# Kernel tuning notes

Measured on AMD Instinct MI355X. Metric: run time of the kernel, lower is better.

The kernel has to match this reference:

```python
import jax, jax.numpy as jnp
import numpy as np
import math

NUM_HEADS = 16
CONSTITUENCY_PENALTY = 0.5
CONSTITUENT_BLOCK = 64  # deterministic stand-in for the ChomskyParser constituency spans


def constituency_penalty_mask(seq_len, dtype):
    # Tokens in the same constituent (contiguous block) attend freely;
    # cross-constituent pairs are penalized by CONSTITUENCY_PENALTY.
    blk = jnp.arange(seq_len) // CONSTITUENT_BLOCK
    return jnp.where(blk[:, None] != blk[None, :], CONSTITUENCY_PENALTY, 0.0).astype(dtype)


def setup_inputs() -> dict:
    key = jax.random.key(0)
    ks = jax.random.split(key, 7)
    B, S, H = 8, 1024, 1024
    scale = 1.0 / math.sqrt(H)
    return {
        "hidden_states": jax.random.normal(ks[0], (B, S, H), jnp.float32),
        "Wq": jax.random.normal(ks[1], (H, H), jnp.float32) * scale,
        "bq": jnp.zeros((H,), jnp.float32),
        "Wk": jax.random.normal(ks[2], (H, H), jnp.float32) * scale,
        "bk": jnp.zeros((H,), jnp.float32),
        "Wv": jax.random.normal(ks[3], (H, H), jnp.float32) * scale,
        "bv": jnp.zeros((H,), jnp.float32),
    }


def reference(hidden_states, Wq, bq, Wk, bk, Wv, bv):
    B, S, H = hidden_states.shape
    nh = NUM_HEADS
    hd = H // nh

    def heads(x):  # [B,S,H] -> [B,nh,S,hd]
        return x.reshape(B, S, nh, hd).transpose(0, 2, 1, 3)

    q = heads(hidden_states @ Wq + bq)
    k = heads(hidden_states @ Wk + bk)
    v = heads(hidden_states @ Wv + bv)

    scores = jnp.einsum("bhqd,bhkd->bhqk", q, k) / jnp.sqrt(jnp.asarray(hd, q.dtype))
    # constituency penalty subtracted before softmax (broadcast over batch, heads)
    scores = scores - constituency_penalty_mask(S, scores.dtype)[None, None, :, :]
    probs = jax.nn.softmax(scores, axis=-1)  # dropout is identity in eval

    ctx = jnp.einsum("bhqk,bhkd->bhqd", probs, v)
    ctx = ctx.transpose(0, 2, 1, 3).reshape(B, S, H)
    return ctx
```

## Files before the change

### kernel.cpp

```cpp
#include <hip/hip_runtime.h>
#include <cstdint>

#define BB 8
#define SQ 1024
#define HH 1024
#define NH 16
#define HD 64

typedef __attribute__((ext_vector_type(4))) float f32x4;
typedef __attribute__((ext_vector_type(8))) __bf16 bf16x8;
typedef __attribute__((ext_vector_type(8))) unsigned short u16x8;
typedef __attribute__((ext_vector_type(4))) unsigned short u16x4;

__device__ __forceinline__ unsigned short f2bf(float f){
  uint32_t u = __builtin_bit_cast(uint32_t, f);
  u += 0x7FFFu + ((u >> 16) & 1u);
  return (unsigned short)(u >> 16);
}

__device__ __forceinline__ void gload_lds16(const void* g, void* l){
  __builtin_amdgcn_global_load_lds((__attribute__((address_space(1))) void*)g,
                                   (__attribute__((address_space(3))) void*)l,
                                   16, 0, 0);
}

__global__ __launch_bounds__(256) void k_convert_x(const float* __restrict__ x,
                                                   unsigned short* __restrict__ xb){
  int i = blockIdx.x * 256 + threadIdx.x;
  const f32x4* xv = (const f32x4*)x;
  f32x4 a = xv[2*i], b = xv[2*i+1];
  u16x8 o;
  o[0]=f2bf(a[0]); o[1]=f2bf(a[1]); o[2]=f2bf(a[2]); o[3]=f2bf(a[3]);
  o[4]=f2bf(b[0]); o[5]=f2bf(b[1]); o[6]=f2bf(b[2]); o[7]=f2bf(b[3]);
  ((u16x8*)xb)[i] = o;
}

__global__ __launch_bounds__(256) void k_wt(const float* __restrict__ Wq,
                                            const float* __restrict__ Wk,
                                            const float* __restrict__ Wv,
                                            unsigned short* __restrict__ wt){
  __shared__ float t[32][33];
  int p = blockIdx.z;
  const float* W = (p==0)?Wq:((p==1)?Wk:Wv);
  int n0 = blockIdx.x*32, k0 = blockIdx.y*32;
  int tx = threadIdx.x, ty = threadIdx.y;
  #pragma unroll
  for(int j=0;j<32;j+=8) t[ty+j][tx] = W[(size_t)(k0+ty+j)*HH + n0+tx];
  __syncthreads();
  unsigned short* o = wt + (size_t)p*HH*HH;
  #pragma unroll
  for(int j=0;j<32;j+=8) o[(size_t)(n0+ty+j)*HH + k0+tx] = f2bf(t[tx][ty+j]);
}

#define BM 128
#define BN 128
#define BK 64
__global__ __launch_bounds__(256) void k_qkv(const unsigned short* __restrict__ Xb,
                                             const unsigned short* __restrict__ Wt,
                                             const float* __restrict__ bq,
                                             const float* __restrict__ bk,
                                             const float* __restrict__ bv,
                                             unsigned short* __restrict__ q_ws,
                                             unsigned short* __restrict__ k_ws,
                                             unsigned short* __restrict__ vt_ws){
  __shared__ __align__(16) unsigned short As[2][BM*BK];
  __shared__ __align__(16) unsigned short Bs[2][BN*BK];
  int tid = threadIdx.x;
  int lane = tid & 63, wid = tid >> 6;
  int bid = blockIdx.x;
  int sw = (bid & 7)*192 + (bid >> 3);
  int nt = sw % 24, mt = sw / 24;
  int m0 = mt*BM, n0 = nt*BN;
  int wm = (wid & 1)*64, wn = (wid >> 1)*64;
  int lr = lane & 15, g = lane >> 4;

  int srow = tid >> 3;
  int sch  = (tid & 7) ^ (srow & 7);

  const f32x4 zf = {0.f,0.f,0.f,0.f};
  f32x4 acc[4][4];
  #pragma unroll
  for(int a=0;a<4;a++)
    #pragma unroll
    for(int b=0;b<4;b++) acc[a][b] = zf;

  #pragma unroll
  for(int it=0; it<4; it++){
    int row = it*32 + srow, slot = it*256 + tid;
    gload_lds16(Xb + (size_t)(m0+row)*1024 + sch*8, &As[0][slot*8]);
    gload_lds16(Wt + (size_t)(n0+row)*1024 + sch*8, &Bs[0][slot*8]);
  }
  __syncthreads();

  int cur = 0;
  for(int kk=0; kk<16; kk++){
    if(kk < 15){
      int kb = (kk+1)*BK;
      #pragma unroll
      for(int it=0; it<4; it++){
        int row = it*32 + srow, slot = it*256 + tid;
        gload_lds16(Xb + (size_t)(m0+row)*1024 + kb + sch*8, &As[cur^1][slot*8]);
        gload_lds16(Wt + (size_t)(n0+row)*1024 + kb + sch*8, &Bs[cur^1][slot*8]);
      }
    }
    #pragma unroll
    for(int ks=0; ks<2; ks++){
      bf16x8 af[4], bfr[4];
      #pragma unroll
      for(int mi=0;mi<4;mi++){
        int r = wm + mi*16 + lr;
        af[mi] = *(const bf16x8*)&As[cur][r*64 + (((ks*4+g) ^ (r&7))<<3)];
      }
      #pragma unroll
      for(int ni=0;ni<4;ni++){
        int r = wn + ni*16 + lr;
        bfr[ni] = *(const bf16x8*)&Bs[cur][r*64 + (((ks*4+g) ^ (r&7))<<3)];
      }
      #pragma unroll
      for(int mi=0;mi<4;mi++)
        #pragma unroll
        for(int ni=0;ni<4;ni++)
          acc[mi][ni] = __builtin_amdgcn_mfma_f32_16x16x32_bf16(af[mi], bfr[ni], acc[mi][ni], 0,0,0);
    }
    __syncthreads();
    cur ^= 1;
  }

  int proj = n0 >> 10;
  const float* bias = (proj==0)?bq:((proj==1)?bk:bv);
  const float QSCALE = 0.18033688f;
  #pragma unroll
  for(int mi=0;mi<4;mi++){
    #pragma unroll
    for(int ni=0;ni<4;ni++){
      int ncol = n0 + wn + ni*16 + lr;
      int hcol = ncol & 1023;
      int h = hcol >> 6, d = hcol & 63;
      float bval = bias[hcol];
      if(proj == 0){
        #pragma unroll
        for(int i=0;i<4;i++){
          int m = m0 + wm + mi*16 + g*4 + i;
          int b = m >> 10, s = m & 1023;
          q_ws[((size_t)(b*NH + h)*SQ + s)*HD + d] = f2bf((acc[mi][ni][i] + bval)*QSCALE);
        }
      } else if(proj == 1){
        #pragma unroll
        for(int i=0;i<4;i++){
          int m = m0 + wm + mi*16 + g*4 + i;
          int b = m >> 10, s = m & 1023;
          k_ws[((size_t)(b*NH + h)*SQ + s)*HD + d] = f2bf(acc[mi][ni][i] + bval);
        }
      } else {
        int m = m0 + wm + mi*16 + g*4;
        int b = m >> 10, s = m & 1023;
        u16x4 pk;
        #pragma unroll
        for(int i=0;i<4;i++) pk[i] = f2bf(acc[mi][ni][i] + bval);
        *(u16x4*)&vt_ws[((size_t)(b*NH + h)*HD + d)*SQ + s] = pk;
      }
    }
  }
}

__global__ __launch_bounds__(256) void k_attn(const unsigned short* __restrict__ q_ws,
                                              const unsigned short* __restrict__ k_ws,
                                              const unsigned short* __restrict__ vt_ws,
                                              float* __restrict__ out){
  __shared__ __align__(16) unsigned short Ks[2][64*64];
  __shared__ __align__(16) unsigned short Vs[2][64*64];
  __shared__ __align__(16) unsigned short Ps[4][32*64];
  int tid = threadIdx.x, lane = tid & 63, wid = tid >> 6;
  int lr = lane & 15, g = lane >> 4;
  int bid = blockIdx.x;
  int swz = (bid & 7)*128 + (bid >> 3);
  int qb = swz & 7, bh = swz >> 3;
  int qw = qb*128 + wid*32;
  const unsigned short* qp = q_ws + (size_t)bh*SQ*HD;
  const unsigned short* kp = k_ws + (size_t)bh*SQ*HD;
  const unsigned short* vp = vt_ws + (size_t)bh*HD*SQ;

  bf16x8 qf[2][2];
  #pragma unroll
  for(int ns=0;ns<2;ns++)
    #pragma unroll
    for(int ks=0;ks<2;ks++)
      qf[ns][ks] = *(const bf16x8*)&qp[(size_t)(qw + ns*16 + lr)*HD + ks*32 + g*8];

  int diag = qw >> 6;

  int srow = tid >> 3;
  int sch  = (tid & 7) ^ (srow & 7);

  const f32x4 zf = {0.f,0.f,0.f,0.f};
  float lacc[2] = {0.f, 0.f};
  f32x4 co[4][2];
  #pragma unroll
  for(int ms=0;ms<4;ms++)
    #pragma unroll
    for(int ns=0;ns<2;ns++) co[ms][ns] = zf;

  unsigned short* Pw = &Ps[wid][0];

  #pragma unroll
  for(int it=0; it<2; it++){
    int row = it*32 + srow, slot = it*256 + tid;
    gload_lds16(kp + (size_t)row*HD + sch*8, &Ks[0][slot*8]);
    gload_lds16(vp + (size_t)row*SQ + sch*8, &Vs[0][slot*8]);
  }
  __syncthreads();

  int cur = 0;
  for(int kt=0; kt<16; kt++){
    if(kt < 15){
      int kb = (kt+1)*64;
      #pragma unroll
      for(int it=0; it<2; it++){
        int row = it*32 + srow, slot = it*256 + tid;
        gload_lds16(kp + (size_t)(kb+row)*HD + sch*8, &Ks[cur^1][slot*8]);
        gload_lds16(vp + (size_t)row*SQ + kb + sch*8, &Vs[cur^1][slot*8]);
      }
    }

    f32x4 sc[4][2];
    #pragma unroll
    for(int ms=0;ms<4;ms++){
      int r = ms*16 + lr;
      bf16x8 kf0 = *(const bf16x8*)&Ks[cur][r*64 + ((g ^ (r&7))<<3)];
      bf16x8 kf1 = *(const bf16x8*)&Ks[cur][r*64 + (((4+g) ^ (r&7))<<3)];
      #pragma unroll
      for(int ns=0;ns<2;ns++){
        sc[ms][ns] = __builtin_amdgcn_mfma_f32_16x16x32_bf16(kf0, qf[ns][0], zf, 0,0,0);
        sc[ms][ns] = __builtin_amdgcn_mfma_f32_16x16x32_bf16(kf1, qf[ns][1], sc[ms][ns], 0,0,0);
      }
    }

    float add = (kt == diag) ? 0.72134752f : 0.0f;

    #pragma unroll
    for(int ms=0;ms<4;ms++){
      #pragma unroll
      for(int ns=0;ns<2;ns++){
        u16x4 pk;
        #pragma unroll
        for(int i=0;i<4;i++){
          float pv = __builtin_amdgcn_exp2f(sc[ms][ns][i] + add);
          lacc[ns] += pv;
          pk[i] = f2bf(pv);
        }
        int q = ns*16 + lr;
        int c = ms*2 + (g>>1);
        *(u16x4*)&Pw[q*64 + ((c ^ (q&7))<<3) + (g&1)*4] = pk;
      }
    }

    #pragma unroll
    for(int ms=0;ms<4;ms++){
      int vr = ms*16 + lr;
      bf16x8 vf0 = *(const bf16x8*)&Vs[cur][vr*64 + ((g ^ (vr&7))<<3)];
      bf16x8 vf1 = *(const bf16x8*)&Vs[cur][vr*64 + (((4+g) ^ (vr&7))<<3)];
      #pragma unroll
      for(int ns=0;ns<2;ns++){
        int q = ns*16 + lr;
        bf16x8 pf0 = *(const bf16x8*)&Pw[q*64 + ((g ^ (q&7))<<3)];
        bf16x8 pf1 = *(const bf16x8*)&Pw[q*64 + (((4+g) ^ (q&7))<<3)];
        co[ms][ns] = __builtin_amdgcn_mfma_f32_16x16x32_bf16(vf0, pf0, co[ms][ns], 0,0,0);
        co[ms][ns] = __builtin_amdgcn_mfma_f32_16x16x32_bf16(vf1, pf1, co[ms][ns], 0,0,0);
      }
    }

    __syncthreads();
    cur ^= 1;
  }

  float rl[2];
  #pragma unroll
  for(int ns=0;ns<2;ns++){
    float l = lacc[ns];
    l += __shfl_xor(l, 16);
    l += __shfl_xor(l, 32);
    rl[ns] = 1.0f / l;
  }
  int b = bh >> 4, h = bh & 15;
  #pragma unroll
  for(int ms=0;ms<4;ms++){
    #pragma unroll
    for(int ns=0;ns<2;ns++){
      int q = qw + ns*16 + lr;
      int d = h*HD + ms*16 + g*4;
      f32x4 r = co[ms][ns];
      r[0]*=rl[ns]; r[1]*=rl[ns]; r[2]*=rl[ns]; r[3]*=rl[ns];
      *(f32x4*)&out[((size_t)(b*SQ + q))*HH + d] = r;
    }
  }
}

extern "C" void kernel_launch(void* const* d_in, const int* in_sizes, int n_in,
                              void* d_out, int out_size, void* d_ws, size_t ws_size,
                              hipStream_t stream){
  const float* hs = (const float*)d_in[0];
  const float* Wq = (const float*)d_in[1];
  const float* bq = (const float*)d_in[2];
  const float* Wk = (const float*)d_in[3];
  const float* bk = (const float*)d_in[4];
  const float* Wv = (const float*)d_in[5];
  const float* bv = (const float*)d_in[6];
  float* out = (float*)d_out;

  unsigned char* ws = (unsigned char*)d_ws;
  const size_t NX = (size_t)8192*1024;
  unsigned short* xb    = (unsigned short*)ws;
  unsigned short* wt    = (unsigned short*)(ws + NX*2);
  unsigned short* q_ws  = (unsigned short*)(ws + NX*2 + (size_t)3*1024*1024*2);
  unsigned short* k_ws  = q_ws + NX;
  unsigned short* vt_ws = k_ws + NX;

  k_convert_x<<<4096, 256, 0, stream>>>(hs, xb);
  k_wt<<<dim3(32,32,3), dim3(32,8), 0, stream>>>(Wq, Wk, Wv, wt);
  k_qkv<<<24*64, 256, 0, stream>>>(xb, wt, bq, bk, bv, q_ws, k_ws, vt_ws);
  k_attn<<<1024, 256, 0, stream>>>(q_ws, k_ws, vt_ws, out);
}
```

Before: 226.4 us.

## Merge prep kernels, single-buffer QKV GEMM, enlarge attention blocks to 512 threads

Fuses the x conversion and weight transpose into one launch so only one kernel-launch gap remains. The QKV GEMM drops its LDS double buffer and block swizzle in favour of a simple load-sync-compute loop, which removes the overlap of global loads with MFMA work. Attention blocks now hold 8 waves covering 256 queries, so each K/V tile loaded into LDS is shared by twice as many waves, and the P fragments are hoisted out of the V loop. The larger blocks halve the attention grid to 512 blocks, which may reduce occupancy and load balance.

```diff
diff --git a/kernel.cpp b/kernel.cpp
--- a/kernel.cpp
+++ b/kernel.cpp
@@ -24,32 +24,35 @@
                                    16, 0, 0);
 }
 
-__global__ __launch_bounds__(256) void k_convert_x(const float* __restrict__ x,
-                                                   unsigned short* __restrict__ xb){
-  int i = blockIdx.x * 256 + threadIdx.x;
-  const f32x4* xv = (const f32x4*)x;
-  f32x4 a = xv[2*i], b = xv[2*i+1];
-  u16x8 o;
-  o[0]=f2bf(a[0]); o[1]=f2bf(a[1]); o[2]=f2bf(a[2]); o[3]=f2bf(a[3]);
-  o[4]=f2bf(b[0]); o[5]=f2bf(b[1]); o[6]=f2bf(b[2]); o[7]=f2bf(b[3]);
-  ((u16x8*)xb)[i] = o;
-}
-
-__global__ __launch_bounds__(256) void k_wt(const float* __restrict__ Wq,
-                                            const float* __restrict__ Wk,
-                                            const float* __restrict__ Wv,
-                                            unsigned short* __restrict__ wt){
+__global__ __launch_bounds__(256) void k_prep(const float* __restrict__ x,
+                                              unsigned short* __restrict__ xb,
+                                              const float* __restrict__ Wq,
+                                              const float* __restrict__ Wk,
+                                              const float* __restrict__ Wv,
+                                              unsigned short* __restrict__ wt){
   __shared__ float t[32][33];
-  int p = blockIdx.z;
-  const float* W = (p==0)?Wq:((p==1)?Wk:Wv);
-  int n0 = blockIdx.x*32, k0 = blockIdx.y*32;
-  int tx = threadIdx.x, ty = threadIdx.y;
-  #pragma unroll
-  for(int j=0;j<32;j+=8) t[ty+j][tx] = W[(size_t)(k0+ty+j)*HH + n0+tx];
-  __syncthreads();
-  unsigned short* o = wt + (size_t)p*HH*HH;
-  #pragma unroll
-  for(int j=0;j<32;j+=8) o[(size_t)(n0+ty+j)*HH + k0+tx] = f2bf(t[tx][ty+j]);
+  int bid = blockIdx.x, tid = threadIdx.x;
+  if(bid < 4096){
+    int i = bid * 256 + tid;
+    const f32x4* xv = (const f32x4*)x;
+    f32x4 a = xv[2*i], b = xv[2*i+1];
+    u16x8 o;
+    o[0]=f2bf(a[0]); o[1]=f2bf(a[1]); o[2]=f2bf(a[2]); o[3]=f2bf(a[3]);
+    o[4]=f2bf(b[0]); o[5]=f2bf(b[1]); o[6]=f2bf(b[2]); o[7]=f2bf(b[3]);
+    ((u16x8*)xb)[i] = o;
+  } else {
+    int idx = bid - 4096;
+    int p = idx >> 10, rem = idx & 1023;
+    const float* W = (p==0)?Wq:((p==1)?Wk:Wv);
+    int n0 = (rem & 31)*32, k0 = (rem >> 5)*32;
+    int tx = tid & 31, ty = tid >> 5;
+    #pragma unroll
+    for(int j=0;j<32;j+=8) t[ty+j][tx] = W[(size_t)(k0+ty+j)*HH + n0+tx];
+    __syncthreads();
+    unsigned short* o = wt + (size_t)p*HH*HH;
+    #pragma unroll
+    for(int j=0;j<32;j+=8) o[(size_t)(n0+ty+j)*HH + k0+tx] = f2bf(t[tx][ty+j]);
+  }
 }
 
 #define BM 128
@@ -63,20 +66,15 @@
                                              unsigned short* __restrict__ q_ws,
                                              unsigned short* __restrict__ k_ws,
                                              unsigned short* __restrict__ vt_ws){
-  __shared__ __align__(16) unsigned short As[2][BM*BK];
-  __shared__ __align__(16) unsigned short Bs[2][BN*BK];
+  __shared__ __align__(16) unsigned short As[BM*BK];
+  __shared__ __align__(16) unsigned short Bs[BN*BK];
   int tid = threadIdx.x;
   int lane = tid & 63, wid = tid >> 6;
-  int bid = blockIdx.x;
-  int sw = (bid & 7)*192 + (bid >> 3);
-  int nt = sw % 24, mt = sw / 24;
+  int nt = blockIdx.x % 24, mt = blockIdx.x / 24;
   int m0 = mt*BM, n0 = nt*BN;
   int wm = (wid & 1)*64, wn = (wid >> 1)*64;
   int lr = lane & 15, g = lane >> 4;
 
-  int srow = tid >> 3;
-  int sch  = (tid & 7) ^ (srow & 7);
-
   const f32x4 zf = {0.f,0.f,0.f,0.f};
   f32x4 acc[4][4];
   #pragma unroll
@@ -84,37 +82,34 @@
     #pragma unroll
     for(int b=0;b<4;b++) acc[a][b] = zf;
 
-  #pragma unroll
-  for(int it=0; it<4; it++){
-    int row = it*32 + srow, slot = it*256 + tid;
-    gload_lds16(Xb + (size_t)(m0+row)*1024 + sch*8, &As[0][slot*8]);
-    gload_lds16(Wt + (size_t)(n0+row)*1024 + sch*8, &Bs[0][slot*8]);
-  }
-  __syncthreads();
-
-  int cur = 0;
-  for(int kk=0; kk<16; kk++){
-    if(kk < 15){
-      int kb = (kk+1)*BK;
-      #pragma unroll
-      for(int it=0; it<4; it++){
-        int row = it*32 + srow, slot = it*256 + tid;
-        gload_lds16(Xb + (size_t)(m0+row)*1024 + kb + sch*8, &As[cur^1][slot*8]);
-        gload_lds16(Wt + (size_t)(n0+row)*1024 + kb + sch*8, &Bs[cur^1][slot*8]);
-      }
-    }
+  for(int kk=0; kk<1024; kk+=BK){
+    __syncthreads();
+    #pragma unroll
+    for(int it=0; it<4; it++){
+      int slot = it*256 + tid;
+      int row = slot >> 3, ch = (slot & 7) ^ (row & 7);
+      gload_lds16(Xb + (size_t)(m0+row)*1024 + kk + ch*8, &As[slot*8]);
+    }
+    #pragma unroll
+    for(int it=0; it<4; it++){
+      int slot = it*256 + tid;
+      int row = slot >> 3, ch = (slot & 7) ^ (row & 7);
+      gload_lds16(Wt + (size_t)(n0+row)*1024 + kk + ch*8, &Bs[slot*8]);
+    }
+    __syncthreads();
+
     #pragma unroll
     for(int ks=0; ks<2; ks++){
       bf16x8 af[4], bfr[4];
       #pragma unroll
       for(int mi=0;mi<4;mi++){
         int r = wm + mi*16 + lr;
-        af[mi] = *(const bf16x8*)&As[cur][r*64 + (((ks*4+g) ^ (r&7))<<3)];
+        af[mi] = *(const bf16x8*)&As[r*64 + (((ks*4+g) ^ (r&7))<<3)];
       }
       #pragma unroll
       for(int ni=0;ni<4;ni++){
         int r = wn + ni*16 + lr;
-        bfr[ni] = *(const bf16x8*)&Bs[cur][r*64 + (((ks*4+g) ^ (r&7))<<3)];
+        bfr[ni] = *(const bf16x8*)&Bs[r*64 + (((ks*4+g) ^ (r&7))<<3)];
       }
       #pragma unroll
       for(int mi=0;mi<4;mi++)
@@ -122,8 +117,6 @@
         for(int ni=0;ni<4;ni++)
           acc[mi][ni] = __builtin_amdgcn_mfma_f32_16x16x32_bf16(af[mi], bfr[ni], acc[mi][ni], 0,0,0);
     }
-    __syncthreads();
-    cur ^= 1;
   }
 
   int proj = n0 >> 10;
@@ -163,19 +156,19 @@
   }
 }
 
-__global__ __launch_bounds__(256) void k_attn(const unsigned short* __restrict__ q_ws,
+__global__ __launch_bounds__(512) void k_attn(const unsigned short* __restrict__ q_ws,
                                               const unsigned short* __restrict__ k_ws,
                                               const unsigned short* __restrict__ vt_ws,
                                               float* __restrict__ out){
   __shared__ __align__(16) unsigned short Ks[2][64*64];
   __shared__ __align__(16) unsigned short Vs[2][64*64];
-  __shared__ __align__(16) unsigned short Ps[4][32*64];
+  __shared__ __align__(16) unsigned short Ps[8][32*64];
   int tid = threadIdx.x, lane = tid & 63, wid = tid >> 6;
   int lr = lane & 15, g = lane >> 4;
   int bid = blockIdx.x;
-  int swz = (bid & 7)*128 + (bid >> 3);
-  int qb = swz & 7, bh = swz >> 3;
-  int qw = qb*128 + wid*32;
+  int swz = (bid & 7)*64 + (bid >> 3);
+  int qb = swz & 3, bh = swz >> 2;
+  int qw = qb*256 + wid*32;
   const unsigned short* qp = q_ws + (size_t)bh*SQ*HD;
   const unsigned short* kp = k_ws + (size_t)bh*SQ*HD;
   const unsigned short* vp = vt_ws + (size_t)bh*HD*SQ;
@@ -202,24 +195,16 @@
 
   unsigned short* Pw = &Ps[wid][0];
 
-  #pragma unroll
-  for(int it=0; it<2; it++){
-    int row = it*32 + srow, slot = it*256 + tid;
-    gload_lds16(kp + (size_t)row*HD + sch*8, &Ks[0][slot*8]);
-    gload_lds16(vp + (size_t)row*SQ + sch*8, &Vs[0][slot*8]);
-  }
+  gload_lds16(kp + (size_t)srow*HD + sch*8, &Ks[0][tid*8]);
+  gload_lds16(vp + (size_t)srow*SQ + sch*8, &Vs[0][tid*8]);
   __syncthreads();
 
   int cur = 0;
   for(int kt=0; kt<16; kt++){
     if(kt < 15){
       int kb = (kt+1)*64;
-      #pragma unroll
-      for(int it=0; it<2; it++){
-        int row = it*32 + srow, slot = it*256 + tid;
-        gload_lds16(kp + (size_t)(kb+row)*HD + sch*8, &Ks[cur^1][slot*8]);
-        gload_lds16(vp + (size_t)row*SQ + kb + sch*8, &Vs[cur^1][slot*8]);
-      }
+      gload_lds16(kp + (size_t)(kb+srow)*HD + sch*8, &Ks[cur^1][tid*8]);
+      gload_lds16(vp + (size_t)srow*SQ + kb + sch*8, &Vs[cur^1][tid*8]);
     }
 
     f32x4 sc[4][2];
@@ -254,6 +239,13 @@
       }
     }
 
+    bf16x8 pf[2][2];
+    #pragma unroll
+    for(int ns=0;ns<2;ns++){
+      int q = ns*16 + lr;
+      pf[ns][0] = *(const bf16x8*)&Pw[q*64 + ((g ^ (q&7))<<3)];
+      pf[ns][1] = *(const bf16x8*)&Pw[q*64 + (((4+g) ^ (q&7))<<3)];
+    }
     #pragma unroll
     for(int ms=0;ms<4;ms++){
       int vr = ms*16 + lr;
@@ -261,11 +253,8 @@
       bf16x8 vf1 = *(const bf16x8*)&Vs[cur][vr*64 + (((4+g) ^ (vr&7))<<3)];
       #pragma unroll
       for(int ns=0;ns<2;ns++){
-        int q = ns*16 + lr;
-        bf16x8 pf0 = *(const bf16x8*)&Pw[q*64 + ((g ^ (q&7))<<3)];
-        bf16x8 pf1 = *(const bf16x8*)&Pw[q*64 + (((4+g) ^ (q&7))<<3)];
-        co[ms][ns] = __builtin_amdgcn_mfma_f32_16x16x32_bf16(vf0, pf0, co[ms][ns], 0,0,0);
-        co[ms][ns] = __builtin_amdgcn_mfma_f32_16x16x32_bf16(vf1, pf1, co[ms][ns], 0,0,0);
+        co[ms][ns] = __builtin_amdgcn_mfma_f32_16x16x32_bf16(vf0, pf[ns][0], co[ms][ns], 0,0,0);
+        co[ms][ns] = __builtin_amdgcn_mfma_f32_16x16x32_bf16(vf1, pf[ns][1], co[ms][ns], 0,0,0);
       }
     }
 
@@ -315,8 +304,7 @@
   unsigned short* k_ws  = q_ws + NX;
   unsigned short* vt_ws = k_ws + NX;
 
-  k_convert_x<<<4096, 256, 0, stream>>>(hs, xb);
-  k_wt<<<dim3(32,32,3), dim3(32,8), 0, stream>>>(Wq, Wk, Wv, wt);
+  k_prep<<<7168, 256, 0, stream>>>(hs, xb, Wq, Wk, Wv, wt);
   k_qkv<<<24*64, 256, 0, stream>>>(xb, wt, bq, bk, bv, q_ws, k_ws, vt_ws);
-  k_attn<<<1024, 256, 0, stream>>>(q_ws, k_ws, vt_ws, out);
-}
+  k_attn<<<512, 512, 0, stream>>>(q_ws, k_ws, vt_ws, out);
+}
```

Result: no change. 223.6 us (-1.3%).
